# Kernel tuning notes

Hardware: AMD Instinct MI355X
Metric: run time of the kernel (lower is better)

The kernel has to match this reference:

```python
import jax, jax.numpy as jnp
import numpy as np


def setup_inputs() -> dict:
    key = jax.random.key(0)
    ks = jax.random.split(key, 6)
    B, T, C = 1, 2048, 2048
    Hq, Hkv = 32, 8
    D = C // Hq  # 64
    s = 0.02  # weight init scale for numerical stability
    return {
        "x": jax.random.normal(ks[0], (B, T, C), dtype=jnp.float32),
        "Wq": jax.random.normal(ks[1], (C, C), dtype=jnp.float32) * s,
        "Wk": jax.random.normal(ks[2], (Hkv * D, C), dtype=jnp.float32) * s,
        "Wv": jax.random.normal(ks[3], (Hkv * D, C), dtype=jnp.float32) * s,
        "Wo": jax.random.normal(ks[4], (C, C), dtype=jnp.float32) * s,
        "bo": jnp.zeros((C,), dtype=jnp.float32),
        "num_query_heads": Hq,
        "num_kv_heads": Hkv,
    }


def reference(x, Wq, Wk, Wv, Wo, bo, num_query_heads, num_kv_heads):
    B, T, C = x.shape
    Hq, Hkv = num_query_heads, num_kv_heads
    D = C // Hq
    G = Hq // Hkv  # queries per kv head

    q = (x @ Wq.T).reshape(B, T, Hkv, G, D)   # grouped query heads
    k = (x @ Wk.T).reshape(B, T, Hkv, D)
    v = (x @ Wv.T).reshape(B, T, Hkv, D)

    scale = 1.0 / jnp.sqrt(jnp.asarray(D, dtype=x.dtype))
    # [B, Hkv, G, T, T]; KV head broadcast over group dim instead of repeat_interleave
    scores = jnp.einsum("bthgd,bshd->bhgts", q, k) * scale

    causal = jnp.tril(jnp.ones((T, T), dtype=bool))  # allow j <= i
    scores = jnp.where(causal, scores, jnp.asarray(-jnp.inf, dtype=scores.dtype))
    attn = jax.nn.softmax(scores, axis=-1)  # dropout is identity at p=0.0 / eval

    out = jnp.einsum("bhgts,bshd->bthgd", attn, v).reshape(B, T, C)
    return out @ Wo.T + bo
```

## Files before the change

kernel.cpp:

```cpp
#include <hip/hip_runtime.h>
#include <hip/hip_bf16.h>

typedef __attribute__((ext_vector_type(8))) short short8;
typedef __attribute__((ext_vector_type(16))) float floatx16;
typedef __attribute__((ext_vector_type(4))) float floatx4;
typedef __attribute__((ext_vector_type(4))) unsigned uintx4;

__device__ __forceinline__ short f2bf(float f) {
    unsigned u = __builtin_bit_cast(unsigned, f);
    u += 0x7fffu + ((u >> 16) & 1u);
    return (short)(u >> 16);
}

__device__ __forceinline__ unsigned pk_bf16(float lo, float hi) {
    unsigned short a = __builtin_bit_cast(unsigned short, (__bf16)lo);
    unsigned short b = __builtin_bit_cast(unsigned short, (__bf16)hi);
    return (unsigned)a | ((unsigned)b << 16);
}

__device__ __forceinline__ void gload_lds16(const void* g, void* l) {
    __builtin_amdgcn_global_load_lds(
        (const __attribute__((address_space(1))) unsigned*)g,
        (__attribute__((address_space(3))) unsigned*)l, 16, 0, 0);
}

__global__ __launch_bounds__(256)
void convsw(const float* __restrict__ src, short* __restrict__ dst) {
    const int row = blockIdx.x;
    const int c = threadIdx.x;
    const int kt = c >> 3, cc = c & 7;
    const float* s = src + (size_t)row * 2048 + kt * 64 + (cc ^ (row & 7)) * 8;
    float4 v0 = *(const float4*)s;
    float4 v1 = *(const float4*)(s + 4);
    short8 o = { f2bf(v0.x), f2bf(v0.y), f2bf(v0.z), f2bf(v0.w),
                 f2bf(v1.x), f2bf(v1.y), f2bf(v1.z), f2bf(v1.w) };
    *(short8*)(dst + (size_t)row * 2048 + kt * 64 + cc * 8) = o;
}

__global__ __launch_bounds__(256)
void conv_all(const float* __restrict__ x, const float* __restrict__ Wq,
              const float* __restrict__ Wk, const float* __restrict__ Wv,
              short* __restrict__ xb, short* __restrict__ wqkv) {
    const int bid = blockIdx.x;
    const float* src; short* dst; int srow, drow;
    if (bid < 2048)      { src = x;  dst = xb;   srow = bid;        drow = bid; }
    else {
        int r = bid - 2048;
        dst = wqkv; drow = r;
        if (r < 2048)      { src = Wq; srow = r; }
        else if (r < 2560) { src = Wk; srow = r - 2048; }
        else               { src = Wv; srow = r - 2560; }
    }
    const int c = threadIdx.x;
    const int kt = c >> 3, cc = c & 7;
    const float* s = src + (size_t)srow * 2048 + kt * 64 + (cc ^ (drow & 7)) * 8;
    float4 v0 = *(const float4*)s;
    float4 v1 = *(const float4*)(s + 4);
    short8 o = { f2bf(v0.x), f2bf(v0.y), f2bf(v0.z), f2bf(v0.w),
                 f2bf(v1.x), f2bf(v1.y), f2bf(v1.z), f2bf(v1.w) };
    *(short8*)(dst + (size_t)drow * 2048 + kt * 64 + cc * 8) = o;
}

template<int BN, int EPI>
__global__ __launch_bounds__(512, 4)
void gemm8(const short* __restrict__ A, const short* __restrict__ Bw,
           short* __restrict__ qb, short* __restrict__ kb, short* __restrict__ vt,
           float* __restrict__ fout, const float* __restrict__ bias) {
    constexpr int K = 2048;
    constexpr int NN = BN / 32;
    constexpr int ACH = 128 * 8;
    constexpr int NCH = (128 + BN) * 8;
    __shared__ short sm[2][(128 + BN) * 64];

    const int t = threadIdx.x, lane = t & 63, w = t >> 6;
    const int wm = w & 3, wn = w >> 2;
    const int l15 = lane & 15, lh = lane >> 4;
    const int bn = blockIdx.x, bm = blockIdx.y;
    const int ra0 = bm * 128;
    const short* Bbase = Bw + (size_t)bn * BN * K;

    floatx4 acc[2][NN] = {};

    auto stage = [&](int buf, int k0) {
        short* base = &sm[buf][0];
        #pragma unroll
        for (int i = 0; i < NCH / 512; ++i) {
            int c = i * 512 + t;
            if (c < ACH) {
                int row = c >> 3, cc = c & 7;
                gload_lds16(A + (size_t)(ra0 + row) * K + k0 + cc * 8, base + c * 8);
            } else {
                int c2 = c - ACH;
                int row = c2 >> 3, cc = c2 & 7;
                gload_lds16(Bbase + (size_t)row * K + k0 + cc * 8, base + (ACH + c2) * 8);
            }
        }
    };

    stage(0, 0);
    #pragma unroll 1
    for (int it = 0; it < K / 64; ++it) {
        __syncthreads();
        if (it + 1 < K / 64) stage((it + 1) & 1, (it + 1) * 64);
        const short* As = &sm[it & 1][0];
        const short* Bs = As + 128 * 64;
        #pragma unroll
        for (int kf = 0; kf < 2; ++kf) {
            short8 a[2], b[NN];
            #pragma unroll
            for (int m = 0; m < 2; ++m) {
                int arow = wm * 32 + m * 16 + l15;
                a[m] = *(const short8*)(As + arow * 64 + (((kf * 4 + lh) ^ (arow & 7)) << 3));
            }
            #pragma unroll
            for (int n = 0; n < NN; ++n) {
                int brow = wn * (BN / 2) + n * 16 + l15;
                b[n] = *(const short8*)(Bs + brow * 64 + (((kf * 4 + lh) ^ (brow & 7)) << 3));
            }
            #pragma unroll
            for (int m = 0; m < 2; ++m)
                #pragma unroll
                for (int n = 0; n < NN; ++n)
                    acc[m][n] = __builtin_amdgcn_mfma_f32_16x16x32_bf16(a[m], b[n], acc[m][n], 0, 0, 0);
        }
    }

    #pragma unroll
    for (int m = 0; m < 2; ++m) {
        #pragma unroll
        for (int n = 0; n < NN; ++n) {
            #pragma unroll
            for (int r = 0; r < 4; ++r) {
                int row = ra0 + wm * 32 + m * 16 + lh * 4 + r;
                int col = bn * BN + wn * (BN / 2) + n * 16 + l15;
                float v = acc[m][n][r];
                if constexpr (EPI == 1) {
                    fout[(size_t)row * 2048 + col] = v + bias[col];
                } else {
                    if (col < 2048) {
                        qb[(size_t)row * 2048 + col] = f2bf(v * 0.18033688011112042f);
                    } else if (col < 2560) {
                        int kcol = col - 2048, within = kcol & 63;
                        int cp = ((within >> 3) ^ (row & 7)) & 7;
                        kb[(size_t)row * 512 + (kcol & ~63) + (cp << 3) + (within & 7)] = f2bf(v);
                    } else {
                        int dg = col - 2560;
                        int cp = (((row >> 3) & 7) ^ (dg & 7)) & 7;
                        vt[(size_t)dg * 2048 + (row & ~63) + (cp << 3) + (row & 7)] = f2bf(v);
                    }
                }
            }
        }
    }
}

__global__ __launch_bounds__(512, 4)
void attn_fwd(const short* __restrict__ qb, const short* __restrict__ kb,
              const short* __restrict__ vt, short* __restrict__ ob) {
    __shared__ __align__(16) short smem[2][16384];

    const int t = threadIdx.x, lane = t & 63, w = t >> 6;
    const int l31 = lane & 31, hi = lane >> 5;
    const int pairi = blockIdx.x;
    const int hq = blockIdx.y, hk = hq >> 2;
    const int qtA = pairi, qtB = 31 - pairi;
    const int a = w >> 1, p = w & 1;
    const int myqt = (a < 2) ? qtA : qtB;
    const int q0 = myqt * 64 + (a & 1) * 32;
    const int rg = q0 + l31;
    const int swl = l31 & 7;

    short8 qf[4];
    {
        const short* qrow = qb + (size_t)rg * 2048 + hq * 64;
        #pragma unroll
        for (int kk = 0; kk < 4; ++kk)
            qf[kk] = *(const short8*)(qrow + kk * 16 + hi * 8);
    }

    float m = -3e38f, l = 0.f;
    floatx16 acc[2] = {};

    auto stage = [&](int buf, int j0) {
        short* base = &smem[buf][0];
        #pragma unroll
        for (int i = 0; i < 4; ++i) {
            int c = i * 512 + t;
            if (i < 2) {
                int row = c >> 3, cc = c & 7;
                gload_lds16(kb + (size_t)(j0 + row) * 512 + hk * 64 + cc * 8, base + c * 8);
            } else {
                int cv = c - 1024, drow = cv >> 4, cc = cv & 15;
                gload_lds16(vt + (size_t)(hk * 64 + drow) * 2048 + j0 + cc * 8, base + c * 8);
            }
        }
    };

    const int nss = (qtB >> 1) + 1;
    stage(0, 0);
    for (int ss = 0; ss < nss; ++ss) {
        __syncthreads();
        if (ss + 1 < nss) stage((ss + 1) & 1, (ss + 1) * 128);
        const int kt = 2 * ss + p;
        if (kt <= myqt) {
            const short* K0 = &smem[ss & 1][0];
            const short* V0 = &smem[ss & 1][8192];

            floatx16 sT[2];
            #pragma unroll
            for (int kb2 = 0; kb2 < 2; ++kb2) {
                floatx16 acc2 = {};
                const int row = p * 64 + kb2 * 32 + l31;
                #pragma unroll
                for (int kk = 0; kk < 4; ++kk) {
                    short8 kf = *(const short8*)(K0 + row * 64 + (((2 * kk + hi) ^ swl) << 3));
                    acc2 = __builtin_amdgcn_mfma_f32_32x32x16_bf16(kf, qf[kk], acc2, 0, 0, 0);
                }
                sT[kb2] = acc2;
            }

            if (kt == myqt) {
                #pragma unroll
                for (int kb2 = 0; kb2 < 2; ++kb2)
                    #pragma unroll
                    for (int r = 0; r < 16; ++r) {
                        int jg = kt * 64 + kb2 * 32 + (r & 3) + 8 * (r >> 2) + 4 * hi;
                        if (jg > rg) sT[kb2][r] = -3e38f;
                    }
            }

            float v[16];
            #pragma unroll
            for (int r = 0; r < 16; ++r) v[r] = fmaxf(sT[0][r], sT[1][r]);
            #pragma unroll
            for (int st = 8; st >= 1; st >>= 1)
                #pragma unroll
                for (int r = 0; r < 8; ++r)
                    if (r < st) v[r] = fmaxf(v[r], v[r + st]);
            float tm = fmaxf(v[0], __shfl_xor(v[0], 32));

            if (!__all(tm <= m + 8.0f)) {
                float mn = fmaxf(m, tm);
                float sf = __builtin_amdgcn_exp2f(m - mn);
                m = mn;
                l *= sf;
                #pragma unroll
                for (int n = 0; n < 2; ++n)
                    #pragma unroll
                    for (int r = 0; r < 16; ++r) acc[n][r] *= sf;
            }

            float sv[16];
            #pragma unroll
            for (int kb2 = 0; kb2 < 2; ++kb2)
                #pragma unroll
                for (int r = 0; r < 16; ++r)
                    sT[kb2][r] = __builtin_amdgcn_exp2f(sT[kb2][r] - m);
            #pragma unroll
            for (int r = 0; r < 16; ++r) sv[r] = sT[0][r] + sT[1][r];
            #pragma unroll
            for (int st = 8; st >= 1; st >>= 1)
                #pragma unroll
                for (int r = 0; r < 8; ++r)
                    if (r < st) sv[r] += sv[r + st];
            l += sv[0] + __shfl_xor(sv[0], 32);

            #pragma unroll
            for (int kb2 = 0; kb2 < 2; ++kb2) {
                unsigned Qd[8], Pd[8];
                #pragma unroll
                for (int c = 0; c < 8; ++c)
                    Qd[c] = pk_bf16(sT[kb2][2 * c], sT[kb2][2 * c + 1]);
                #pragma unroll
                for (int c = 0; c < 8; ++c)
                    Pd[c] = __shfl_xor(Qd[c], 32);
                #pragma unroll
                for (int b = 0; b < 2; ++b) {
                    uintx4 j;
                    if (b == 0) {
                        j.x = hi ? Pd[2] : Qd[0];
                        j.y = hi ? Pd[3] : Qd[1];
                        j.z = hi ? Qd[2] : Pd[0];
                        j.w = hi ? Qd[3] : Pd[1];
                    } else {
                        j.x = hi ? Pd[6] : Qd[4];
                        j.y = hi ? Pd[7] : Qd[5];
                        j.z = hi ? Qd[6] : Pd[4];
                        j.w = hi ? Qd[7] : Pd[5];
                    }
                    short8 pf = __builtin_bit_cast(short8, j);
                    const int kk = kb2 * 2 + b;
                    const int ch = p * 64 + (((2 * kk + hi) ^ swl) << 3);
                    short8 vf0 = *(const short8*)(V0 + l31 * 128 + ch);
                    acc[0] = __builtin_amdgcn_mfma_f32_32x32x16_bf16(vf0, pf, acc[0], 0, 0, 0);
                    short8 vf1 = *(const short8*)(V0 + (32 + l31) * 128 + ch);
                    acc[1] = __builtin_amdgcn_mfma_f32_32x32x16_bf16(vf1, pf, acc[1], 0, 0, 0);
                }
            }
        }
    }

    __syncthreads();
    float* mb = (float*)&smem[0][0] + ((size_t)a * 64 + lane) * 34;
    if (p == 1) {
        #pragma unroll
        for (int n = 0; n < 2; ++n)
            #pragma unroll
            for (int r = 0; r < 16; ++r) mb[n * 16 + r] = acc[n][r];
        mb[32] = m;
        mb[33] = l;
    }
    __syncthreads();
    if (p == 0) {
        const float m1 = mb[32], l1 = mb[33];
        const float M = fmaxf(m, m1);
        const float sf0 = __builtin_amdgcn_exp2f(m - M);
        const float sf1 = __builtin_amdgcn_exp2f(m1 - M);
        const float linv = 1.0f / (sf0 * l + sf1 * l1);
        const int sw8 = rg & 7;
        #pragma unroll
        for (int n = 0; n < 2; ++n) {
            #pragma unroll
            for (int g = 0; g < 4; ++g) {
                #pragma unroll
                for (int e = 0; e < 4; e += 2) {
                    int r = 4 * g + e;
                    float o0 = (sf0 * acc[n][r]     + sf1 * mb[n * 16 + r])     * linv;
                    float o1 = (sf0 * acc[n][r + 1] + sf1 * mb[n * 16 + r + 1]) * linv;
                    unsigned pkv = pk_bf16(o0, o1);
                    int d = 32 * n + e + 8 * g + 4 * hi;
                    int col = hq * 64 + d;
                    int cp = ((col >> 3) & 7) ^ sw8;
                    *(unsigned*)(ob + (size_t)rg * 2048 + (col & ~63) + (cp << 3) + (col & 7)) = pkv;
                }
            }
        }
    }
}

extern "C" void kernel_launch(void* const* d_in, const int* in_sizes, int n_in,
                              void* d_out, int out_size, void* d_ws, size_t ws_size,
                              hipStream_t stream) {
    const float* x  = (const float*)d_in[0];
    const float* Wq = (const float*)d_in[1];
    const float* Wk = (const float*)d_in[2];
    const float* Wv = (const float*)d_in[3];
    const float* Wo = (const float*)d_in[4];
    const float* bo = (const float*)d_in[5];

    char* ws = (char*)d_ws;
    short* xb   = (short*)ws;
    short* wqkv = (short*)(ws + ((size_t)8  << 20));
    short* qb   = (short*)(ws + ((size_t)20 << 20));
    short* kb   = (short*)(ws + ((size_t)28 << 20));
    short* vt   = (short*)(ws + ((size_t)30 << 20));
    short* ob   = xb;
    short* wob  = wqkv;

    conv_all<<<5120, 256, 0, stream>>>(x, Wq, Wk, Wv, xb, wqkv);
    gemm8<128, 0><<<dim3(24, 16), 512, 0, stream>>>(xb, wqkv, qb, kb, vt, nullptr, nullptr);
    convsw<<<2048, 256, 0, stream>>>(Wo, wob);
    attn_fwd<<<dim3(16, 32), 512, 0, stream>>>(qb, kb, vt, ob);
    gemm8<64, 1><<<dim3(32, 16), 512, 0, stream>>>(ob, wob, nullptr, nullptr, nullptr,
                                                   (float*)d_out, bo);
}
```

Measured before the change: 122.4 us.

## Rebalance paired-tile attention so idle warps help the longer causal tile

Previously the warps handling the short tile A went idle once their causal range was done, while the tile-B warps kept iterating. Now, after tile A finishes, those warps write out A, reload Q for tile B, and split the remaining KV blocks with the B warps, each taking one 32-key half of every 64-key subtile. A final four-way merge of the softmax partial states goes through LDS. This is meant to remove the load imbalance inside each block, at the cost of extra merge steps, more syncs and a staging overlap with the scratch buffer.

Result: no change. 122.0 us (-0.3%).

```diff
diff --git a/kernel.cpp b/kernel.cpp
--- a/kernel.cpp
+++ b/kernel.cpp
@@ -5,6 +5,8 @@
 typedef __attribute__((ext_vector_type(16))) float floatx16;
 typedef __attribute__((ext_vector_type(4))) float floatx4;
 typedef __attribute__((ext_vector_type(4))) unsigned uintx4;
+
+template<int N> struct IC { static constexpr int v = N; };
 
 __device__ __forceinline__ short f2bf(float f) {
     unsigned u = __builtin_bit_cast(unsigned, f);
@@ -165,10 +167,11 @@
     const int hq = blockIdx.y, hk = hq >> 2;
     const int qtA = pairi, qtB = 31 - pairi;
     const int a = w >> 1, p = w & 1;
-    const int myqt = (a < 2) ? qtA : qtB;
-    const int q0 = myqt * 64 + (a & 1) * 32;
-    const int rg = q0 + l31;
+    const int s = a & 1, h = a >> 1;
+    const int tile1 = (a < 2) ? qtA : qtB;
     const int swl = l31 & 7;
+
+    int rg = tile1 * 64 + s * 32 + l31;
 
     short8 qf[4];
     {
@@ -196,128 +199,30 @@
         }
     };
 
-    const int nss = (qtB >> 1) + 1;
-    stage(0, 0);
-    for (int ss = 0; ss < nss; ++ss) {
-        __syncthreads();
-        if (ss + 1 < nss) stage((ss + 1) & 1, (ss + 1) * 128);
-        const int kt = 2 * ss + p;
-        if (kt <= myqt) {
-            const short* K0 = &smem[ss & 1][0];
-            const short* V0 = &smem[ss & 1][8192];
-
-            floatx16 sT[2];
-            #pragma unroll
-            for (int kb2 = 0; kb2 < 2; ++kb2) {
-                floatx16 acc2 = {};
-                const int row = p * 64 + kb2 * 32 + l31;
-                #pragma unroll
-                for (int kk = 0; kk < 4; ++kk) {
-                    short8 kf = *(const short8*)(K0 + row * 64 + (((2 * kk + hi) ^ swl) << 3));
-                    acc2 = __builtin_amdgcn_mfma_f32_32x32x16_bf16(kf, qf[kk], acc2, 0, 0, 0);
-                }
-                sT[kb2] = acc2;
-            }
-
-            if (kt == myqt) {
-                #pragma unroll
-                for (int kb2 = 0; kb2 < 2; ++kb2)
-                    #pragma unroll
-                    for (int r = 0; r < 16; ++r) {
-                        int jg = kt * 64 + kb2 * 32 + (r & 3) + 8 * (r >> 2) + 4 * hi;
-                        if (jg > rg) sT[kb2][r] = -3e38f;
-                    }
-            }
-
-            float v[16];
-            #pragma unroll
-            for (int r = 0; r < 16; ++r) v[r] = fmaxf(sT[0][r], sT[1][r]);
-            #pragma unroll
-            for (int st = 8; st >= 1; st >>= 1)
-                #pragma unroll
-                for (int r = 0; r < 8; ++r)
-                    if (r < st) v[r] = fmaxf(v[r], v[r + st]);
-            float tm = fmaxf(v[0], __shfl_xor(v[0], 32));
-
-            if (!__all(tm <= m + 8.0f)) {
-                float mn = fmaxf(m, tm);
-                float sf = __builtin_amdgcn_exp2f(m - mn);
-                m = mn;
-                l *= sf;
-                #pragma unroll
-                for (int n = 0; n < 2; ++n)
-                    #pragma unroll
-                    for (int r = 0; r < 16; ++r) acc[n][r] *= sf;
-            }
-
-            float sv[16];
-            #pragma unroll
-            for (int kb2 = 0; kb2 < 2; ++kb2)
-                #pragma unroll
-                for (int r = 0; r < 16; ++r)
-                    sT[kb2][r] = __builtin_amdgcn_exp2f(sT[kb2][r] - m);
-            #pragma unroll
-            for (int r = 0; r < 16; ++r) sv[r] = sT[0][r] + sT[1][r];
-            #pragma unroll
-            for (int st = 8; st >= 1; st >>= 1)
-                #pragma unroll
-                for (int r = 0; r < 8; ++r)
-                    if (r < st) sv[r] += sv[r + st];
-            l += sv[0] + __shfl_xor(sv[0], 32);
-
-            #pragma unroll
-            for (int kb2 = 0; kb2 < 2; ++kb2) {
-                unsigned Qd[8], Pd[8];
-                #pragma unroll
-                for (int c = 0; c < 8; ++c)
-                    Qd[c] = pk_bf16(sT[kb2][2 * c], sT[kb2][2 * c + 1]);
-                #pragma unroll
-                for (int c = 0; c < 8; ++c)
-                    Pd[c] = __shfl_xor(Qd[c], 32);
-                #pragma unroll
-                for (int b = 0; b < 2; ++b) {
-                    uintx4 j;
-                    if (b == 0) {
-                        j.x = hi ? Pd[2] : Qd[0];
-                        j.y = hi ? Pd[3] : Qd[1];
-                        j.z = hi ? Qd[2] : Pd[0];
-                        j.w = hi ? Qd[3] : Pd[1];
-                    } else {
-                        j.x = hi ? Pd[6] : Qd[4];
-                        j.y = hi ? Pd[7] : Qd[5];
-                        j.z = hi ? Qd[6] : Pd[4];
-                        j.w = hi ? Qd[7] : Pd[5];
-                    }
-                    short8 pf = __builtin_bit_cast(short8, j);
-                    const int kk = kb2 * 2 + b;
-                    const int ch = p * 64 + (((2 * kk + hi) ^ swl) << 3);
-                    short8 vf0 = *(const short8*)(V0 + l31 * 128 + ch);
-                    acc[0] = __builtin_amdgcn_mfma_f32_32x32x16_bf16(vf0, pf, acc[0], 0, 0, 0);
-                    short8 vf1 = *(const short8*)(V0 + (32 + l31) * 128 + ch);
-                    acc[1] = __builtin_amdgcn_mfma_f32_32x32x16_bf16(vf1, pf, acc[1], 0, 0, 0);
-                }
-            }
-        }
-    }
-
-    __syncthreads();
-    float* mb = (float*)&smem[0][0] + ((size_t)a * 64 + lane) * 34;
-    if (p == 1) {
+    auto save_part = [&](float* mb) {
         #pragma unroll
         for (int n = 0; n < 2; ++n)
             #pragma unroll
             for (int r = 0; r < 16; ++r) mb[n * 16 + r] = acc[n][r];
         mb[32] = m;
         mb[33] = l;
-    }
-    __syncthreads();
-    if (p == 0) {
-        const float m1 = mb[32], l1 = mb[33];
-        const float M = fmaxf(m, m1);
-        const float sf0 = __builtin_amdgcn_exp2f(m - M);
-        const float sf1 = __builtin_amdgcn_exp2f(m1 - M);
-        const float linv = 1.0f / (sf0 * l + sf1 * l1);
-        const int sw8 = rg & 7;
+    };
+    auto merge_part = [&](const float* mb) {
+        float m1 = mb[32], l1 = mb[33];
+        float M = fmaxf(m, m1);
+        float sf0 = __builtin_amdgcn_exp2f(m - M);
+        float sf1 = __builtin_amdgcn_exp2f(m1 - M);
+        l = sf0 * l + sf1 * l1;
+        #pragma unroll
+        for (int n = 0; n < 2; ++n)
+            #pragma unroll
+            for (int r = 0; r < 16; ++r)
+                acc[n][r] = sf0 * acc[n][r] + sf1 * mb[n * 16 + r];
+        m = M;
+    };
+    auto writeout = [&](int rgw) {
+        const float linv = 1.0f / l;
+        const int sw8 = rgw & 7;
         #pragma unroll
         for (int n = 0; n < 2; ++n) {
             #pragma unroll
@@ -325,16 +230,170 @@
                 #pragma unroll
                 for (int e = 0; e < 4; e += 2) {
                     int r = 4 * g + e;
-                    float o0 = (sf0 * acc[n][r]     + sf1 * mb[n * 16 + r])     * linv;
-                    float o1 = (sf0 * acc[n][r + 1] + sf1 * mb[n * 16 + r + 1]) * linv;
-                    unsigned pkv = pk_bf16(o0, o1);
+                    unsigned pkv = pk_bf16(acc[n][r] * linv, acc[n][r + 1] * linv);
                     int d = 32 * n + e + 8 * g + 4 * hi;
                     int col = hq * 64 + d;
                     int cp = ((col >> 3) & 7) ^ sw8;
-                    *(unsigned*)(ob + (size_t)rg * 2048 + (col & ~63) + (cp << 3) + (col & 7)) = pkv;
+                    *(unsigned*)(ob + (size_t)rgw * 2048 + (col & ~63) + (cp << 3) + (col & 7)) = pkv;
                 }
             }
         }
+    };
+
+    auto process = [&](const short* K0, const short* V0, int blk0, auto NB,
+                       int kt, bool diag) {
+        constexpr int nblk = decltype(NB)::v;
+        floatx16 sT[nblk];
+        #pragma unroll
+        for (int ib = 0; ib < nblk; ++ib) {
+            floatx16 a2 = {};
+            const int row = p * 64 + (blk0 + ib) * 32 + l31;
+            #pragma unroll
+            for (int kk = 0; kk < 4; ++kk) {
+                short8 kf = *(const short8*)(K0 + row * 64 + (((2 * kk + hi) ^ swl) << 3));
+                a2 = __builtin_amdgcn_mfma_f32_32x32x16_bf16(kf, qf[kk], a2, 0, 0, 0);
+            }
+            sT[ib] = a2;
+        }
+        if (diag) {
+            #pragma unroll
+            for (int ib = 0; ib < nblk; ++ib)
+                #pragma unroll
+                for (int r = 0; r < 16; ++r) {
+                    int jg = kt * 64 + (blk0 + ib) * 32 + (r & 3) + 8 * (r >> 2) + 4 * hi;
+                    if (jg > rg) sT[ib][r] = -3e38f;
+                }
+        }
+        float v[16];
+        #pragma unroll
+        for (int r = 0; r < 16; ++r) {
+            v[r] = sT[0][r];
+            if constexpr (nblk == 2) v[r] = fmaxf(v[r], sT[1][r]);
+        }
+        #pragma unroll
+        for (int st = 8; st >= 1; st >>= 1)
+            #pragma unroll
+            for (int r = 0; r < 8; ++r)
+                if (r < st) v[r] = fmaxf(v[r], v[r + st]);
+        float tm = fmaxf(v[0], __shfl_xor(v[0], 32));
+
+        if (!__all(tm <= m + 8.0f)) {
+            float mn = fmaxf(m, tm);
+            float sf = __builtin_amdgcn_exp2f(m - mn);
+            m = mn;
+            l *= sf;
+            #pragma unroll
+            for (int n = 0; n < 2; ++n)
+                #pragma unroll
+                for (int r = 0; r < 16; ++r) acc[n][r] *= sf;
+        }
+
+        float sv[16];
+        #pragma unroll
+        for (int ib = 0; ib < nblk; ++ib)
+            #pragma unroll
+            for (int r = 0; r < 16; ++r)
+                sT[ib][r] = __builtin_amdgcn_exp2f(sT[ib][r] - m);
+        #pragma unroll
+        for (int r = 0; r < 16; ++r) {
+            sv[r] = sT[0][r];
+            if constexpr (nblk == 2) sv[r] += sT[1][r];
+        }
+        #pragma unroll
+        for (int st = 8; st >= 1; st >>= 1)
+            #pragma unroll
+            for (int r = 0; r < 8; ++r)
+                if (r < st) sv[r] += sv[r + st];
+        l += sv[0] + __shfl_xor(sv[0], 32);
+
+        #pragma unroll
+        for (int ib = 0; ib < nblk; ++ib) {
+            unsigned Qd[8], Pd[8];
+            #pragma unroll
+            for (int c = 0; c < 8; ++c)
+                Qd[c] = pk_bf16(sT[ib][2 * c], sT[ib][2 * c + 1]);
+            #pragma unroll
+            for (int c = 0; c < 8; ++c)
+                Pd[c] = __shfl_xor(Qd[c], 32);
+            #pragma unroll
+            for (int b = 0; b < 2; ++b) {
+                uintx4 j;
+                if (b == 0) {
+                    j.x = hi ? Pd[2] : Qd[0];
+                    j.y = hi ? Pd[3] : Qd[1];
+                    j.z = hi ? Qd[2] : Pd[0];
+                    j.w = hi ? Qd[3] : Pd[1];
+                } else {
+                    j.x = hi ? Pd[6] : Qd[4];
+                    j.y = hi ? Pd[7] : Qd[5];
+                    j.z = hi ? Qd[6] : Pd[4];
+                    j.w = hi ? Qd[7] : Pd[5];
+                }
+                short8 pf = __builtin_bit_cast(short8, j);
+                const int kk = (blk0 + ib) * 2 + b;
+                const int ch = p * 64 + (((2 * kk + hi) ^ swl) << 3);
+                short8 vf0 = *(const short8*)(V0 + l31 * 128 + ch);
+                acc[0] = __builtin_amdgcn_mfma_f32_32x32x16_bf16(vf0, pf, acc[0], 0, 0, 0);
+                short8 vf1 = *(const short8*)(V0 + (32 + l31) * 128 + ch);
+                acc[1] = __builtin_amdgcn_mfma_f32_32x32x16_bf16(vf1, pf, acc[1], 0, 0, 0);
+            }
+        }
+    };
+
+    const int ss_tr = (qtA >> 1) + 1;
+    const int nss = (qtB >> 1) + 1;
+
+    stage(0, 0);
+    for (int ss = 0; ss < ss_tr; ++ss) {
+        __syncthreads();
+        if (ss + 1 < ss_tr) stage((ss + 1) & 1, (ss + 1) * 128);
+        const int kt = 2 * ss + p;
+        if (kt <= tile1)
+            process(&smem[ss & 1][0], &smem[ss & 1][8192], 0, IC<2>{}, kt, kt == tile1);
+    }
+
+    __syncthreads();
+    stage(ss_tr & 1, ss_tr * 128);
+    {
+        float* msc = (float*)&smem[(ss_tr - 1) & 1][0];
+        if (a < 2 && p == 1) save_part(msc + (s * 64 + lane) * 34);
+        __syncthreads();
+        if (a < 2 && p == 0) {
+            merge_part(msc + (s * 64 + lane) * 34);
+            writeout(rg);
+        }
+        if (a < 2) {
+            rg = qtB * 64 + s * 32 + l31;
+            const short* qrow = qb + (size_t)rg * 2048 + hq * 64;
+            #pragma unroll
+            for (int kk = 0; kk < 4; ++kk)
+                qf[kk] = *(const short8*)(qrow + kk * 16 + hi * 8);
+            m = -3e38f;
+            l = 0.f;
+            acc[0] = (floatx16){};
+            acc[1] = (floatx16){};
+        }
+    }
+
+    for (int ss = ss_tr; ss < nss; ++ss) {
+        __syncthreads();
+        if (ss + 1 < nss) stage((ss + 1) & 1, (ss + 1) * 128);
+        const int kt = 2 * ss + p;
+        if (kt <= qtB)
+            process(&smem[ss & 1][0], &smem[ss & 1][8192], h, IC<1>{}, kt, kt == qtB);
+    }
+
+    __syncthreads();
+    float* msc = (float*)&smem[0][0];
+    if (p == 1) save_part(msc + (a * 64 + lane) * 34);
+    __syncthreads();
+    if (p == 0) merge_part(msc + (a * 64 + lane) * 34);
+    __syncthreads();
+    if (p == 0 && a >= 2) save_part(msc + ((a & 1) * 64 + lane) * 34);
+    __syncthreads();
+    if (p == 0 && a < 2) {
+        merge_part(msc + (a * 64 + lane) * 34);
+        writeout(rg);
     }
 }
 
```

## Rebalance attention across warps with split-K partials and direct global K/V loads

Applied to the files above, without the earlier changes.

The attention kernel stops staging K/V tiles through shared memory. Instead, each of the 8 warps takes an equal contiguous slice of the 66 key-tile units for a paired causal query-tile block and reads K and V fragments directly from global memory. Partial softmax states are stored as bf16 in LDS slots and merged by designated warps, which removes the idle warps and per-tile barriers of the old two-way split. The Wo conversion is folded into the single conversion kernel, and K/V are written unswizzled. The trade-offs are uncached repeated global loads of K/V per warp and reduced precision in the partial accumulators.

Measured after the change: 167.4 us. 36.8% more time.

```diff
diff --git a/kernel.cpp b/kernel.cpp
--- a/kernel.cpp
+++ b/kernel.cpp
@@ -25,32 +25,20 @@
 }
 
 __global__ __launch_bounds__(256)
-void convsw(const float* __restrict__ src, short* __restrict__ dst) {
-    const int row = blockIdx.x;
-    const int c = threadIdx.x;
-    const int kt = c >> 3, cc = c & 7;
-    const float* s = src + (size_t)row * 2048 + kt * 64 + (cc ^ (row & 7)) * 8;
-    float4 v0 = *(const float4*)s;
-    float4 v1 = *(const float4*)(s + 4);
-    short8 o = { f2bf(v0.x), f2bf(v0.y), f2bf(v0.z), f2bf(v0.w),
-                 f2bf(v1.x), f2bf(v1.y), f2bf(v1.z), f2bf(v1.w) };
-    *(short8*)(dst + (size_t)row * 2048 + kt * 64 + cc * 8) = o;
-}
-
-__global__ __launch_bounds__(256)
 void conv_all(const float* __restrict__ x, const float* __restrict__ Wq,
               const float* __restrict__ Wk, const float* __restrict__ Wv,
-              short* __restrict__ xb, short* __restrict__ wqkv) {
+              const float* __restrict__ Wo, short* __restrict__ xb,
+              short* __restrict__ wqkv, short* __restrict__ wob) {
     const int bid = blockIdx.x;
     const float* src; short* dst; int srow, drow;
-    if (bid < 2048)      { src = x;  dst = xb;   srow = bid;        drow = bid; }
-    else {
+    if (bid < 2048)      { src = x;  dst = xb;  srow = bid;        drow = bid; }
+    else if (bid < 5120) {
         int r = bid - 2048;
         dst = wqkv; drow = r;
         if (r < 2048)      { src = Wq; srow = r; }
         else if (r < 2560) { src = Wk; srow = r - 2048; }
         else               { src = Wv; srow = r - 2560; }
-    }
+    } else               { src = Wo; dst = wob; srow = bid - 5120; drow = srow; }
     const int c = threadIdx.x;
     const int kt = c >> 3, cc = c & 7;
     const float* s = src + (size_t)srow * 2048 + kt * 64 + (cc ^ (drow & 7)) * 8;
@@ -70,6 +58,7 @@
     constexpr int NN = BN / 32;
     constexpr int ACH = 128 * 8;
     constexpr int NCH = (128 + BN) * 8;
+    constexpr int NIT = K / 64;
     __shared__ short sm[2][(128 + BN) * 64];
 
     const int t = threadIdx.x, lane = t & 63, w = t >> 6;
@@ -99,9 +88,9 @@
 
     stage(0, 0);
     #pragma unroll 1
-    for (int it = 0; it < K / 64; ++it) {
+    for (int it = 0; it < NIT; ++it) {
         __syncthreads();
-        if (it + 1 < K / 64) stage((it + 1) & 1, (it + 1) * 64);
+        if (it + 1 < NIT) stage((it + 1) & 1, (it + 1) * 64);
         const short* As = &sm[it & 1][0];
         const short* Bs = As + 128 * 64;
         #pragma unroll
@@ -140,13 +129,9 @@
                     if (col < 2048) {
                         qb[(size_t)row * 2048 + col] = f2bf(v * 0.18033688011112042f);
                     } else if (col < 2560) {
-                        int kcol = col - 2048, within = kcol & 63;
-                        int cp = ((within >> 3) ^ (row & 7)) & 7;
-                        kb[(size_t)row * 512 + (kcol & ~63) + (cp << 3) + (within & 7)] = f2bf(v);
+                        kb[(size_t)row * 512 + (col - 2048)] = f2bf(v);
                     } else {
-                        int dg = col - 2560;
-                        int cp = (((row >> 3) & 7) ^ (dg & 7)) & 7;
-                        vt[(size_t)dg * 2048 + (row & ~63) + (cp << 3) + (row & 7)] = f2bf(v);
+                        vt[(size_t)(col - 2560) * 2048 + row] = f2bf(v);
                     }
                 }
             }
@@ -157,167 +142,204 @@
 __global__ __launch_bounds__(512, 4)
 void attn_fwd(const short* __restrict__ qb, const short* __restrict__ kb,
               const short* __restrict__ vt, short* __restrict__ ob) {
-    __shared__ __align__(16) short smem[2][16384];
+    __shared__ __align__(16) unsigned slots[10][64][20];
 
     const int t = threadIdx.x, lane = t & 63, w = t >> 6;
     const int l31 = lane & 31, hi = lane >> 5;
-    const int pairi = blockIdx.x;
-    const int hq = blockIdx.y, hk = hq >> 2;
+    const int bid = blockIdx.x;
+    const int pairi = bid >> 5;
+    const int hq = bid & 31;
+    const int hk = hq >> 2;
     const int qtA = pairi, qtB = 31 - pairi;
-    const int a = w >> 1, p = w & 1;
-    const int myqt = (a < 2) ? qtA : qtB;
-    const int q0 = myqt * 64 + (a & 1) * 32;
-    const int rg = q0 + l31;
-    const int swl = l31 & 7;
-
-    short8 qf[4];
-    {
-        const short* qrow = qb + (size_t)rg * 2048 + hq * 64;
-        #pragma unroll
-        for (int kk = 0; kk < 4; ++kk)
-            qf[kk] = *(const short8*)(qrow + kk * 16 + hi * 8);
-    }
+    const int nA = qtA + 1;
+
+    const int start = (w * 66) >> 3;
+    const int end = ((w + 1) * 66) >> 3;
 
     float m = -3e38f, l = 0.f;
     floatx16 acc[2] = {};
-
-    auto stage = [&](int buf, int j0) {
-        short* base = &smem[buf][0];
-        #pragma unroll
-        for (int i = 0; i < 4; ++i) {
-            int c = i * 512 + t;
-            if (i < 2) {
-                int row = c >> 3, cc = c & 7;
-                gload_lds16(kb + (size_t)(j0 + row) * 512 + hk * 64 + cc * 8, base + c * 8);
-            } else {
-                int cv = c - 1024, drow = cv >> 4, cc = cv & 15;
-                gload_lds16(vt + (size_t)(hk * 64 + drow) * 2048 + j0 + cc * 8, base + c * 8);
-            }
-        }
+    short8 qf[4];
+    int rg = 0;
+
+    auto save_part = [&](unsigned* mb) {
+        #pragma unroll
+        for (int n = 0; n < 2; ++n)
+            #pragma unroll
+            for (int r = 0; r < 16; r += 2)
+                mb[n * 8 + (r >> 1)] = pk_bf16(acc[n][r], acc[n][r + 1]);
+        mb[16] = __builtin_bit_cast(unsigned, m);
+        mb[17] = __builtin_bit_cast(unsigned, l);
     };
-
-    const int nss = (qtB >> 1) + 1;
-    stage(0, 0);
-    for (int ss = 0; ss < nss; ++ss) {
-        __syncthreads();
-        if (ss + 1 < nss) stage((ss + 1) & 1, (ss + 1) * 128);
-        const int kt = 2 * ss + p;
-        if (kt <= myqt) {
-            const short* K0 = &smem[ss & 1][0];
-            const short* V0 = &smem[ss & 1][8192];
-
-            floatx16 sT[2];
-            #pragma unroll
-            for (int kb2 = 0; kb2 < 2; ++kb2) {
-                floatx16 acc2 = {};
-                const int row = p * 64 + kb2 * 32 + l31;
+    auto merge_part = [&](const unsigned* mb) {
+        float m1 = __builtin_bit_cast(float, mb[16]);
+        float l1 = __builtin_bit_cast(float, mb[17]);
+        float M = fmaxf(m, m1);
+        float sf0 = __builtin_amdgcn_exp2f(m - M);
+        float sf1 = __builtin_amdgcn_exp2f(m1 - M);
+        l = sf0 * l + sf1 * l1;
+        #pragma unroll
+        for (int n = 0; n < 2; ++n)
+            #pragma unroll
+            for (int r = 0; r < 16; r += 2) {
+                unsigned pk = mb[n * 8 + (r >> 1)];
+                float lo = __builtin_bit_cast(float, pk << 16);
+                float hv = __builtin_bit_cast(float, pk & 0xffff0000u);
+                acc[n][r]     = sf0 * acc[n][r]     + sf1 * lo;
+                acc[n][r + 1] = sf0 * acc[n][r + 1] + sf1 * hv;
+            }
+        m = M;
+    };
+
+    int prev_tag = -1;
+    #pragma unroll 1
+    for (int u = start; u < end; ++u) {
+        const int seq = (u >= 33) ? 1 : 0;
+        const int v = u - (seq ? 33 : 0);
+        const int isB = (v > qtA) ? 1 : 0;
+        const int tile = isB ? qtB : qtA;
+        const int kt = isB ? v - nA : v;
+        const int tag = (seq << 1) | isB;
+        if (tag != prev_tag) {
+            if (prev_tag >= 0) {
+                save_part(&slots[8 + seq][lane][0]);
+                m = -3e38f; l = 0.f;
+                acc[0] = (floatx16){}; acc[1] = (floatx16){};
+            }
+            prev_tag = tag;
+            rg = tile * 64 + seq * 32 + l31;
+            const short* qrow = qb + (size_t)rg * 2048 + hq * 64;
+            #pragma unroll
+            for (int kk = 0; kk < 4; ++kk)
+                qf[kk] = *(const short8*)(qrow + kk * 16 + hi * 8);
+        }
+
+        const short* kbase = kb + (size_t)(kt * 64 + l31) * 512 + hk * 64 + hi * 8;
+        short8 kf0[4], kf1[4];
+        #pragma unroll
+        for (int kk = 0; kk < 4; ++kk) kf0[kk] = *(const short8*)(kbase + kk * 16);
+        #pragma unroll
+        for (int kk = 0; kk < 4; ++kk) kf1[kk] = *(const short8*)(kbase + 32 * 512 + kk * 16);
+        floatx16 sT[2];
+        {
+            floatx16 s0 = {}, s1 = {};
+            __builtin_amdgcn_s_setprio(1);
+            #pragma unroll
+            for (int kk = 0; kk < 4; ++kk) {
+                s0 = __builtin_amdgcn_mfma_f32_32x32x16_bf16(kf0[kk], qf[kk], s0, 0, 0, 0);
+                s1 = __builtin_amdgcn_mfma_f32_32x32x16_bf16(kf1[kk], qf[kk], s1, 0, 0, 0);
+            }
+            __builtin_amdgcn_s_setprio(0);
+            sT[0] = s0; sT[1] = s1;
+        }
+
+        if (kt == tile) {
+            #pragma unroll
+            for (int ib = 0; ib < 2; ++ib)
                 #pragma unroll
-                for (int kk = 0; kk < 4; ++kk) {
-                    short8 kf = *(const short8*)(K0 + row * 64 + (((2 * kk + hi) ^ swl) << 3));
-                    acc2 = __builtin_amdgcn_mfma_f32_32x32x16_bf16(kf, qf[kk], acc2, 0, 0, 0);
+                for (int r = 0; r < 16; ++r) {
+                    int jg = kt * 64 + ib * 32 + (r & 3) + 8 * (r >> 2) + 4 * hi;
+                    if (jg > rg) sT[ib][r] = -3e38f;
                 }
-                sT[kb2] = acc2;
-            }
-
-            if (kt == myqt) {
+        }
+
+        float vr[16];
+        #pragma unroll
+        for (int r = 0; r < 16; ++r) vr[r] = fmaxf(sT[0][r], sT[1][r]);
+        #pragma unroll
+        for (int st = 8; st >= 1; st >>= 1)
+            #pragma unroll
+            for (int r = 0; r < 8; ++r)
+                if (r < st) vr[r] = fmaxf(vr[r], vr[r + st]);
+        float tm = fmaxf(vr[0], __shfl_xor(vr[0], 32));
+
+        if (!__all(tm <= m + 8.0f)) {
+            float mn = fmaxf(m, tm);
+            float sf = __builtin_amdgcn_exp2f(m - mn);
+            m = mn;
+            l *= sf;
+            #pragma unroll
+            for (int n = 0; n < 2; ++n)
                 #pragma unroll
-                for (int kb2 = 0; kb2 < 2; ++kb2)
-                    #pragma unroll
-                    for (int r = 0; r < 16; ++r) {
-                        int jg = kt * 64 + kb2 * 32 + (r & 3) + 8 * (r >> 2) + 4 * hi;
-                        if (jg > rg) sT[kb2][r] = -3e38f;
-                    }
-            }
-
-            float v[16];
-            #pragma unroll
-            for (int r = 0; r < 16; ++r) v[r] = fmaxf(sT[0][r], sT[1][r]);
-            #pragma unroll
-            for (int st = 8; st >= 1; st >>= 1)
-                #pragma unroll
-                for (int r = 0; r < 8; ++r)
-                    if (r < st) v[r] = fmaxf(v[r], v[r + st]);
-            float tm = fmaxf(v[0], __shfl_xor(v[0], 32));
-
-            if (!__all(tm <= m + 8.0f)) {
-                float mn = fmaxf(m, tm);
-                float sf = __builtin_amdgcn_exp2f(m - mn);
-                m = mn;
-                l *= sf;
-                #pragma unroll
-                for (int n = 0; n < 2; ++n)
-                    #pragma unroll
-                    for (int r = 0; r < 16; ++r) acc[n][r] *= sf;
-            }
-
-            float sv[16];
-            #pragma unroll
-            for (int kb2 = 0; kb2 < 2; ++kb2)
-                #pragma unroll
-                for (int r = 0; r < 16; ++r)
-                    sT[kb2][r] = __builtin_amdgcn_exp2f(sT[kb2][r] - m);
-            #pragma unroll
-            for (int r = 0; r < 16; ++r) sv[r] = sT[0][r] + sT[1][r];
-            #pragma unroll
-            for (int st = 8; st >= 1; st >>= 1)
-                #pragma unroll
-                for (int r = 0; r < 8; ++r)
-                    if (r < st) sv[r] += sv[r + st];
-            l += sv[0] + __shfl_xor(sv[0], 32);
-
-            #pragma unroll
-            for (int kb2 = 0; kb2 < 2; ++kb2) {
-                unsigned Qd[8], Pd[8];
-                #pragma unroll
-                for (int c = 0; c < 8; ++c)
-                    Qd[c] = pk_bf16(sT[kb2][2 * c], sT[kb2][2 * c + 1]);
-                #pragma unroll
-                for (int c = 0; c < 8; ++c)
-                    Pd[c] = __shfl_xor(Qd[c], 32);
-                #pragma unroll
-                for (int b = 0; b < 2; ++b) {
-                    uintx4 j;
-                    if (b == 0) {
-                        j.x = hi ? Pd[2] : Qd[0];
-                        j.y = hi ? Pd[3] : Qd[1];
-                        j.z = hi ? Qd[2] : Pd[0];
-                        j.w = hi ? Qd[3] : Pd[1];
-                    } else {
-                        j.x = hi ? Pd[6] : Qd[4];
-                        j.y = hi ? Pd[7] : Qd[5];
-                        j.z = hi ? Qd[6] : Pd[4];
-                        j.w = hi ? Qd[7] : Pd[5];
-                    }
-                    short8 pf = __builtin_bit_cast(short8, j);
-                    const int kk = kb2 * 2 + b;
-                    const int ch = p * 64 + (((2 * kk + hi) ^ swl) << 3);
-                    short8 vf0 = *(const short8*)(V0 + l31 * 128 + ch);
-                    acc[0] = __builtin_amdgcn_mfma_f32_32x32x16_bf16(vf0, pf, acc[0], 0, 0, 0);
-                    short8 vf1 = *(const short8*)(V0 + (32 + l31) * 128 + ch);
-                    acc[1] = __builtin_amdgcn_mfma_f32_32x32x16_bf16(vf1, pf, acc[1], 0, 0, 0);
+                for (int r = 0; r < 16; ++r) acc[n][r] *= sf;
+        }
+
+        const short* vbase = vt + (size_t)(hk * 64 + l31) * 2048 + kt * 64 + hi * 8;
+        short8 vf0[4], vf1[4];
+        #pragma unroll
+        for (int kk = 0; kk < 4; ++kk) vf0[kk] = *(const short8*)(vbase + kk * 16);
+        #pragma unroll
+        for (int kk = 0; kk < 4; ++kk) vf1[kk] = *(const short8*)(vbase + (size_t)32 * 2048 + kk * 16);
+
+        float sv[16];
+        #pragma unroll
+        for (int ib = 0; ib < 2; ++ib)
+            #pragma unroll
+            for (int r = 0; r < 16; ++r)
+                sT[ib][r] = __builtin_amdgcn_exp2f(sT[ib][r] - m);
+        #pragma unroll
+        for (int r = 0; r < 16; ++r) sv[r] = sT[0][r] + sT[1][r];
+        #pragma unroll
+        for (int st = 8; st >= 1; st >>= 1)
+            #pragma unroll
+            for (int r = 0; r < 8; ++r)
+                if (r < st) sv[r] += sv[r + st];
+        l += sv[0] + __shfl_xor(sv[0], 32);
+
+        #pragma unroll
+        for (int ib = 0; ib < 2; ++ib) {
+            unsigned Qd[8], Pd[8];
+            #pragma unroll
+            for (int c = 0; c < 8; ++c)
+                Qd[c] = pk_bf16(sT[ib][2 * c], sT[ib][2 * c + 1]);
+            #pragma unroll
+            for (int c = 0; c < 8; ++c)
+                Pd[c] = __shfl_xor(Qd[c], 32);
+            __builtin_amdgcn_s_setprio(1);
+            #pragma unroll
+            for (int b = 0; b < 2; ++b) {
+                uintx4 j;
+                if (b == 0) {
+                    j.x = hi ? Pd[2] : Qd[0];
+                    j.y = hi ? Pd[3] : Qd[1];
+                    j.z = hi ? Qd[2] : Pd[0];
+                    j.w = hi ? Qd[3] : Pd[1];
+                } else {
+                    j.x = hi ? Pd[6] : Qd[4];
+                    j.y = hi ? Pd[7] : Qd[5];
+                    j.z = hi ? Qd[6] : Pd[4];
+                    j.w = hi ? Qd[7] : Pd[5];
                 }
-            }
+                short8 pf = __builtin_bit_cast(short8, j);
+                const int kk = ib * 2 + b;
+                acc[0] = __builtin_amdgcn_mfma_f32_32x32x16_bf16(vf0[kk], pf, acc[0], 0, 0, 0);
+                acc[1] = __builtin_amdgcn_mfma_f32_32x32x16_bf16(vf1[kk], pf, acc[1], 0, 0, 0);
+            }
+            __builtin_amdgcn_s_setprio(0);
         }
     }
 
+    save_part(&slots[w][lane][0]);
     __syncthreads();
-    float* mb = (float*)&smem[0][0] + ((size_t)a * 64 + lane) * 34;
-    if (p == 1) {
-        #pragma unroll
-        for (int n = 0; n < 2; ++n)
-            #pragma unroll
-            for (int r = 0; r < 16; ++r) mb[n * 16 + r] = acc[n][r];
-        mb[32] = m;
-        mb[33] = l;
-    }
-    __syncthreads();
-    if (p == 0) {
-        const float m1 = mb[32], l1 = mb[33];
-        const float M = fmaxf(m, m1);
-        const float sf0 = __builtin_amdgcn_exp2f(m - M);
-        const float sf1 = __builtin_amdgcn_exp2f(m1 - M);
-        const float linv = 1.0f / (sf0 * l + sf1 * l1);
-        const int sw8 = rg & 7;
+
+    int myTag = (w == 0) ? 0 : (w == 3) ? 1 : (w == 4) ? 2 : (w == 7) ? 3 : -1;
+    if (myTag >= 0) {
+        m = -3e38f; l = 0.f;
+        acc[0] = (floatx16){}; acc[1] = (floatx16){};
+        #pragma unroll
+        for (int w8 = 0; w8 < 8; ++w8) {
+            int uu = ((w8 + 1) * 66) / 8 - 1;
+            int sq = (uu >= 33) ? 1 : 0;
+            int vv = uu - (sq ? 33 : 0);
+            int tg = (sq << 1) | ((vv > qtA) ? 1 : 0);
+            if (tg == myTag) merge_part(&slots[w8][lane][0]);
+        }
+        if (!(myTag & 1) && (nA & 7) && nA < 16)
+            merge_part(&slots[8 + (myTag >> 1)][lane][0]);
+
+        const int s = myTag >> 1, isB = myTag & 1;
+        const int rgw = (isB ? qtB : qtA) * 64 + s * 32 + l31;
+        const float linv = 1.0f / l;
+        const int sw8 = rgw & 7;
         #pragma unroll
         for (int n = 0; n < 2; ++n) {
             #pragma unroll
@@ -325,13 +347,11 @@
                 #pragma unroll
                 for (int e = 0; e < 4; e += 2) {
                     int r = 4 * g + e;
-                    float o0 = (sf0 * acc[n][r]     + sf1 * mb[n * 16 + r])     * linv;
-                    float o1 = (sf0 * acc[n][r + 1] + sf1 * mb[n * 16 + r + 1]) * linv;
-                    unsigned pkv = pk_bf16(o0, o1);
+                    unsigned pkv = pk_bf16(acc[n][r] * linv, acc[n][r + 1] * linv);
                     int d = 32 * n + e + 8 * g + 4 * hi;
                     int col = hq * 64 + d;
                     int cp = ((col >> 3) & 7) ^ sw8;
-                    *(unsigned*)(ob + (size_t)rg * 2048 + (col & ~63) + (cp << 3) + (col & 7)) = pkv;
+                    *(unsigned*)(ob + (size_t)rgw * 2048 + (col & ~63) + (cp << 3) + (col & 7)) = pkv;
                 }
             }
         }
@@ -354,13 +374,12 @@
     short* qb   = (short*)(ws + ((size_t)20 << 20));
     short* kb   = (short*)(ws + ((size_t)28 << 20));
     short* vt   = (short*)(ws + ((size_t)30 << 20));
+    short* wob  = (short*)(ws + ((size_t)32 << 20));
     short* ob   = xb;
-    short* wob  = wqkv;
-
-    conv_all<<<5120, 256, 0, stream>>>(x, Wq, Wk, Wv, xb, wqkv);
+
+    conv_all<<<7168, 256, 0, stream>>>(x, Wq, Wk, Wv, Wo, xb, wqkv, wob);
     gemm8<128, 0><<<dim3(24, 16), 512, 0, stream>>>(xb, wqkv, qb, kb, vt, nullptr, nullptr);
-    convsw<<<2048, 256, 0, stream>>>(Wo, wob);
-    attn_fwd<<<dim3(16, 32), 512, 0, stream>>>(qb, kb, vt, ob);
+    attn_fwd<<<512, 512, 0, stream>>>(qb, kb, vt, ob);
     gemm8<64, 1><<<dim3(32, 16), 512, 0, stream>>>(ob, wob, nullptr, nullptr, nullptr,
                                                    (float*)d_out, bo);
 }
```
